# Kernel tuning notes

Hardware: AMD Instinct MI355X
Metric: run time of the kernel (lower is better)

Reference implementation:

```python
import jax, jax.numpy as jnp
import numpy as np

NUM_HEADS = 8
NUM_GROUPS = 32
EPS = 1e-5


def setup_inputs() -> dict:
    key = jax.random.key(0)
    ks = jax.random.split(key, 6)
    C = 512
    scale = 1.0 / np.sqrt(C)
    return {
        "q": jax.random.normal(ks[0], (2, C, 64, 64), dtype=jnp.float32),
        "gn_w": jnp.ones((C,), jnp.float32),
        "gn_b": jnp.zeros((C,), jnp.float32),
        "wq": jax.random.normal(ks[1], (C, C), jnp.float32) * scale,
        "bq": jnp.zeros((C,), jnp.float32),
        "wk": jax.random.normal(ks[2], (C, C), jnp.float32) * scale,
        "bk": jnp.zeros((C,), jnp.float32),
        "wv": jax.random.normal(ks[3], (C, C), jnp.float32) * scale,
        "bv": jnp.zeros((C,), jnp.float32),
        "wo": jax.random.normal(ks[4], (C, C), jnp.float32) * scale,
        "bo": jnp.zeros((C,), jnp.float32),
    }


def _group_norm(x, w, b):
    # x: [B, C, H, W]
    B, C, H, W = x.shape
    xg = x.reshape(B, NUM_GROUPS, C // NUM_GROUPS, H, W)
    mean = xg.mean(axis=(2, 3, 4), keepdims=True)
    var = xg.var(axis=(2, 3, 4), keepdims=True)
    xn = ((xg - mean) * jax.lax.rsqrt(var + EPS)).reshape(B, C, H, W)
    return xn * w[None, :, None, None] + b[None, :, None, None]


def reference(q, gn_w, gn_b, wq, bq, wk, bk, wv, bv, wo, bo):
    B, C, H, W = q.shape
    hd = C // NUM_HEADS
    resid = q
    x = _group_norm(q, gn_w, gn_b)
    x = x.reshape(B, C, H * W).transpose(0, 2, 1)  # [B, N, C]
    # torch Linear: y = x @ W.T + b  (self-attention: k = v = x)
    qp = x @ wq.T + bq
    kp = x @ wk.T + bk
    vp = x @ wv.T + bv
    N = H * W
    def split(t):  # [B, N, C] -> [B, h, N, hd]
        return t.reshape(B, N, NUM_HEADS, hd).transpose(0, 2, 1, 3)
    qh, kh, vh = split(qp), split(kp), split(vp)
    scores = jnp.einsum('bhnc,bhmc->bhnm', qh, kh) / jnp.sqrt(jnp.float32(hd))
    attn = jax.nn.softmax(scores, axis=-1)
    out = jnp.einsum('bhnm,bhmc->bhnc', attn, vh)
    out = out.transpose(0, 2, 1, 3).reshape(B, N, C)
    out = out @ wo.T + bo
    out2d = out.transpose(0, 2, 1).reshape(B, C, H, W)
    return out2d + resid
```

## Files before the change

kernel.cpp:

```cpp
#include <hip/hip_runtime.h>
#include <hip/hip_bf16.h>
#include <cstdint>
#include <cstddef>

using bf16x8   = __attribute__((ext_vector_type(8))) short;
using f32x4    = __attribute__((ext_vector_type(4))) float;
using f32x16   = __attribute__((ext_vector_type(16))) float;
using ushort8  = __attribute__((ext_vector_type(8))) unsigned short;
using ushort4v = __attribute__((ext_vector_type(4))) unsigned short;
using float4v  = __attribute__((ext_vector_type(4))) float;

#define MFMA16(a,b,c) __builtin_amdgcn_mfma_f32_16x16x32_bf16((a),(b),(c),0,0,0)
#define MFMA32(a,b,c) __builtin_amdgcn_mfma_f32_32x32x16_bf16((a),(b),(c),0,0,0)

#define QSCALE 0.18033688011112042f

__device__ __forceinline__ unsigned short f2bf(float f){
    union { float f; unsigned u; } v; v.f = f;
    unsigned r = v.u + 0x7FFFu + ((v.u >> 16) & 1u);
    return (unsigned short)(r >> 16);
}

__device__ __forceinline__ int cvtpk(float lo, float hi){
    int r;
    asm volatile("v_cvt_pk_bf16_f32 %0, %1, %2" : "=v"(r) : "v"(lo), "v"(hi));
    return r;
}

#if __has_builtin(__builtin_amdgcn_permlane32_swap)
__device__ __forceinline__ void plswap(int &a, int &b){
    auto r = __builtin_amdgcn_permlane32_swap(a, b, false, false);
    a = r[0]; b = r[1];
}
#else
__device__ __forceinline__ void plswap(int &a, int &b){
    int ta = __shfl_xor(a, 32), tb = __shfl_xor(b, 32);
    bool hi = ((threadIdx.x & 63) >= 32);
    int na = hi ? tb : a;
    int nb = hi ? b  : ta;
    a = na; b = nb;
}
#endif

__device__ __forceinline__ void gload16(const unsigned short* g, unsigned short* l){
    __builtin_amdgcn_global_load_lds(
        (const __attribute__((address_space(1))) void*)g,
        (__attribute__((address_space(3))) void*)l,
        16, 0, 0);
}

__global__ __launch_bounds__(256) void gn_stats_wconv(const float* __restrict__ x,
                                                      float* __restrict__ mean,
                                                      float* __restrict__ rstd,
                                                      const float* __restrict__ w0, const float* __restrict__ w1,
                                                      const float* __restrict__ w2, const float* __restrict__ w3,
                                                      unsigned short* wqk, unsigned short* wv, unsigned short* wo){
    int bid = blockIdx.x;
    if (bid < 64){
        int bg = bid;
        const float4v* p4 = (const float4v*)(x + (size_t)bg * 65536);
        float s = 0.f, ss = 0.f;
        for (int i = threadIdx.x; i < 16384; i += 256){
            float4v v = p4[i];
            s  += v[0]+v[1]+v[2]+v[3];
            ss += v[0]*v[0]+v[1]*v[1]+v[2]*v[2]+v[3]*v[3];
        }
        __shared__ float ls[4], lss[4];
        int lane = threadIdx.x & 63, w = threadIdx.x >> 6;
        #pragma unroll
        for (int o = 32; o > 0; o >>= 1){ s += __shfl_down(s, o); ss += __shfl_down(ss, o); }
        if (lane == 0){ ls[w] = s; lss[w] = ss; }
        __syncthreads();
        if (threadIdx.x == 0){
            float S = ls[0]+ls[1]+ls[2]+ls[3];
            float SS = lss[0]+lss[1]+lss[2]+lss[3];
            float m = S * (1.f/65536.f);
            float var = SS * (1.f/65536.f) - m*m;
            mean[bg] = m;
            rstd[bg] = rsqrtf(var + 1e-5f);
        }
    } else {
        int i2 = bid - 64;
        int y = i2 >> 8, bx = i2 & 255;
        const float* src; unsigned short* dst; float sc = 1.0f;
        switch (y){
            case 0: src = w0; dst = wqk;          sc = QSCALE; break;
            case 1: src = w1; dst = wqk + 512*512; break;
            case 2: src = w2; dst = wv; break;
            default: src = w3; dst = wo; break;
        }
        int i = (bx*256 + threadIdx.x) * 4;
        float4v v = *(const float4v*)(src + i);
        ushort4v o;
        #pragma unroll
        for (int j = 0; j < 4; j++) o[j] = f2bf(v[j]*sc);
        *(ushort4v*)(dst + i) = o;
    }
}

__global__ __launch_bounds__(256) void gn_apply(const float* __restrict__ x,
                                                const float* __restrict__ mean,
                                                const float* __restrict__ rstd,
                                                const float* __restrict__ gw,
                                                const float* __restrict__ gb,
                                                unsigned short* __restrict__ xn){
    int b = blockIdx.z, c0 = blockIdx.y * 64, n0 = blockIdx.x * 64;
    __shared__ unsigned short tile[64][68];
    for (int i = threadIdx.x; i < 64*16; i += 256){
        int row = i >> 4, f4 = i & 15;
        int c = c0 + row;
        int g = b*32 + (c >> 4);
        float rs = rstd[g];
        float wgt = gw[c] * rs;
        float bia = gb[c] - mean[g] * wgt;
        float4v v = *(const float4v*)(x + ((size_t)(b*512 + c))*4096 + n0 + f4*4);
        ushort4v o;
        #pragma unroll
        for (int j = 0; j < 4; j++) o[j] = f2bf(v[j]*wgt + bia);
        *(ushort4v*)&tile[row][f4*4] = o;
    }
    __syncthreads();
    for (int i = threadIdx.x; i < 64*8; i += 256){
        int nr = i >> 3, c8 = i & 7;
        ushort8 o;
        #pragma unroll
        for (int j = 0; j < 8; j++) o[j] = tile[c8*8 + j][nr];
        *(ushort8*)(xn + ((size_t)(b*4096 + n0 + nr))*512 + c0 + c8*8) = o;
    }
}

__global__ __launch_bounds__(256) void gemm_qkv(const unsigned short* __restrict__ xn,
                                                const unsigned short* __restrict__ wqk,
                                                const unsigned short* __restrict__ Wv,
                                                const float* __restrict__ bq,
                                                const float* __restrict__ bk,
                                                const float* __restrict__ bv,
                                                unsigned short* __restrict__ Q,
                                                unsigned short* __restrict__ K,
                                                unsigned short* __restrict__ Vt){
    __shared__ unsigned short Al[128*32];
    __shared__ unsigned short Bl[128*32];
    int bid = blockIdx.x;
    int t = threadIdx.x, lane = t & 63, w = t >> 6;
    int wr = w >> 1, wc = w & 1;
    int lr = lane >> 2, lc = lane & 3;

    if (bid < 512){
        int m0 = (bid & 63) * 128, n0 = (bid >> 6) * 128;
        f32x4 acc[4][4] = {};
        const unsigned short* Asrc = xn  + (size_t)(m0 + w*32 + lr)*512 + lc*8;
        const unsigned short* Bsrc = wqk + (size_t)(n0 + w*32 + lr)*512 + lc*8;
        unsigned short* Adst = &Al[(w*32)*32];
        unsigned short* Bdst = &Bl[(w*32)*32];

        for (int ks = 0; ks < 16; ks++){
            gload16(Asrc + ks*32,          Adst);
            gload16(Asrc + ks*32 + 16*512, Adst + 16*32);
            gload16(Bsrc + ks*32,          Bdst);
            gload16(Bsrc + ks*32 + 16*512, Bdst + 16*32);
            asm volatile("s_waitcnt vmcnt(0)" ::: "memory");
            __syncthreads();
            bf16x8 a[4], b[4];
            #pragma unroll
            for (int mi = 0; mi < 4; mi++) a[mi] = *(bf16x8*)&Al[(wr*64 + mi*16 + (lane&15))*32 + (lane>>4)*8];
            #pragma unroll
            for (int ni = 0; ni < 4; ni++) b[ni] = *(bf16x8*)&Bl[(wc*64 + ni*16 + (lane&15))*32 + (lane>>4)*8];
            #pragma unroll
            for (int mi = 0; mi < 4; mi++)
                #pragma unroll
                for (int ni = 0; ni < 4; ni++)
                    acc[mi][ni] = MFMA16(a[mi], b[ni], acc[mi][ni]);
            __syncthreads();
        }

        int cK = n0 >> 9;
        const float* bias = cK ? bk : bq;
        unsigned short* dst0 = cK ? K : Q;
        float bsc = cK ? 1.0f : QSCALE;
        #pragma unroll
        for (int mi = 0; mi < 4; mi++)
            #pragma unroll
            for (int ni = 0; ni < 4; ni++)
                #pragma unroll
                for (int r = 0; r < 4; r++){
                    int mrow = m0 + wr*64 + mi*16 + (lane>>4)*4 + r;
                    int col  = (n0 & 511) + wc*64 + ni*16 + (lane&15);
                    int b_ = mrow >> 12, n = mrow & 4095;
                    int h = col >> 6, d = col & 63;
                    float v = acc[mi][ni][r] + bias[col]*bsc;
                    dst0[(size_t)((b_*8+h)*4096 + n)*64 + d] = f2bf(v);
                }
    } else {
        int i2 = bid - 512;
        int m0 = (i2 & 7) * 64, n0 = (i2 >> 3) * 128;
        f32x4 acc[2][4] = {};
        const unsigned short* Asrc = Wv + (size_t)(m0 + w*16 + lr)*512 + lc*8;
        const unsigned short* Bsrc = xn + (size_t)(n0 + w*32 + lr)*512 + lc*8;
        unsigned short* Adst = &Al[(w*16)*32];
        unsigned short* Bdst = &Bl[(w*32)*32];

        for (int ks = 0; ks < 16; ks++){
            gload16(Asrc + ks*32,          Adst);
            gload16(Bsrc + ks*32,          Bdst);
            gload16(Bsrc + ks*32 + 16*512, Bdst + 16*32);
            asm volatile("s_waitcnt vmcnt(0)" ::: "memory");
            __syncthreads();
            bf16x8 a[2], b[4];
            #pragma unroll
            for (int mi = 0; mi < 2; mi++) a[mi] = *(bf16x8*)&Al[(wr*32 + mi*16 + (lane&15))*32 + (lane>>4)*8];
            #pragma unroll
            for (int ni = 0; ni < 4; ni++) b[ni] = *(bf16x8*)&Bl[(wc*64 + ni*16 + (lane&15))*32 + (lane>>4)*8];
            #pragma unroll
            for (int mi = 0; mi < 2; mi++)
                #pragma unroll
                for (int ni = 0; ni < 4; ni++)
                    acc[mi][ni] = MFMA16(a[mi], b[ni], acc[mi][ni]);
            __syncthreads();
        }
        #pragma unroll
        for (int mi = 0; mi < 2; mi++)
            #pragma unroll
            for (int ni = 0; ni < 4; ni++)
                #pragma unroll
                for (int r = 0; r < 4; r++){
                    int row  = m0 + wr*32 + mi*16 + (lane>>4)*4 + r;
                    int colm = n0 + wc*64 + ni*16 + (lane&15);
                    int b_ = colm >> 12, n = colm & 4095;
                    int h = row >> 6, d = row & 63;
                    float v = acc[mi][ni][r] + bv[row];
                    Vt[(size_t)((b_*8+h)*64 + d)*4096 + n] = f2bf(v);
                }
    }
}

__global__ __launch_bounds__(256) void gemm_o2(const unsigned short* __restrict__ Wo,
                                               const unsigned short* __restrict__ Om,
                                               const float* __restrict__ bo,
                                               const float* __restrict__ resid,
                                               float* __restrict__ outp){
    __shared__ unsigned short Al[64*32];
    __shared__ unsigned short Bl[128*32];
    int t = threadIdx.x, lane = t & 63, w = t >> 6;
    int wr = w >> 1, wc = w & 1;
    int m0 = blockIdx.x * 64, n0 = blockIdx.y * 128;
    int lr = lane >> 2, lc = lane & 3;
    f32x4 acc[2][4] = {};

    const unsigned short* Asrc = Wo + (size_t)(m0 + w*16 + lr)*512 + lc*8;
    const unsigned short* Bsrc = Om + (size_t)(n0 + w*32 + lr)*512 + lc*8;
    unsigned short* Adst = &Al[(w*16)*32];
    unsigned short* Bdst = &Bl[(w*32)*32];

    for (int ks = 0; ks < 16; ks++){
        gload16(Asrc + ks*32,          Adst);
        gload16(Bsrc + ks*32,          Bdst);
        gload16(Bsrc + ks*32 + 16*512, Bdst + 16*32);
        asm volatile("s_waitcnt vmcnt(0)" ::: "memory");
        __syncthreads();
        bf16x8 a[2], b[4];
        #pragma unroll
        for (int mi = 0; mi < 2; mi++) a[mi] = *(bf16x8*)&Al[(wr*32 + mi*16 + (lane&15))*32 + (lane>>4)*8];
        #pragma unroll
        for (int ni = 0; ni < 4; ni++) b[ni] = *(bf16x8*)&Bl[(wc*64 + ni*16 + (lane&15))*32 + (lane>>4)*8];
        #pragma unroll
        for (int mi = 0; mi < 2; mi++)
            #pragma unroll
            for (int ni = 0; ni < 4; ni++)
                acc[mi][ni] = MFMA16(a[mi], b[ni], acc[mi][ni]);
        __syncthreads();
    }
    #pragma unroll
    for (int mi = 0; mi < 2; mi++)
        #pragma unroll
        for (int ni = 0; ni < 4; ni++)
            #pragma unroll
            for (int r = 0; r < 4; r++){
                int row  = m0 + wr*32 + mi*16 + (lane>>4)*4 + r;
                int colm = n0 + wc*64 + ni*16 + (lane&15);
                int b_ = colm >> 12, n = colm & 4095;
                size_t oi = ((size_t)(b_*512 + row))*4096 + n;
                outp[oi] = acc[mi][ni][r] + bo[row] + resid[oi];
            }
}

__global__ __launch_bounds__(128, 2) void attn5(const unsigned short* __restrict__ Q,
                                                const unsigned short* __restrict__ K,
                                                const unsigned short* __restrict__ Vt,
                                                unsigned short* __restrict__ O){
    int bid = blockIdx.x;
    int idx = bid >> 3;
    int bh = ((bid & 7) << 1) | (idx >> 6);
    int qt = idx & 63;
    int t = threadIdx.x, lane = t & 63, w = t >> 6;
    int ln = lane & 31, hi = lane >> 5;
    int q0 = qt * 64;

    __shared__ unsigned short Kl[2][64*64];
    __shared__ unsigned short Vl[2][64*64];

    const unsigned short* Qb = Q  + (size_t)bh * 4096 * 64;
    const unsigned short* Kb = K  + (size_t)bh * 4096 * 64;
    const unsigned short* Vb = Vt + (size_t)bh * 64 * 4096;

    bf16x8 bqa[4], bqb[4];
    #pragma unroll
    for (int dsub = 0; dsub < 4; dsub++){
        bqa[dsub] = *(const bf16x8*)(Qb + (size_t)(q0 + ln)*64      + dsub*16 + hi*8);
        bqb[dsub] = *(const bf16x8*)(Qb + (size_t)(q0 + 32 + ln)*64 + dsub*16 + hi*8);
    }

    int srow = lane >> 3;
    int sswz = (lane & 7) ^ srow;

    auto stage = [&](int buf, int kt){
        int kv0 = kt * 64;
        #pragma unroll
        for (int i = 0; i < 4; i++){
            int r0 = w*32 + i*8;
            gload16(Kb + (size_t)(kv0 + r0 + srow)*64 + sswz*8, &Kl[buf][r0*64]);
        }
        #pragma unroll
        for (int i = 0; i < 4; i++){
            int r0 = w*32 + i*8;
            gload16(Vb + (size_t)(r0 + srow)*4096 + kv0 + sswz*8, &Vl[buf][r0*64]);
        }
    };

    stage(0, 0);

    f32x16 o0a, o1a, o0b, o1b, z;
    #pragma unroll
    for (int r = 0; r < 16; r++){ o0a[r]=0.f; o1a[r]=0.f; o0b[r]=0.f; o1b[r]=0.f; z[r]=0.f; }
    float lsA = 0.f, lsB = 0.f;

    const char* KbA = (const char*)&Kl[0][0] + (w*32 + ln)*128;
    const char* VbA = (const char*)&Vl[0][0] + ln*128;
    int swzr = (ln & 7) << 4;

    for (int kt = 0; kt < 64; kt++){
        asm volatile("s_waitcnt vmcnt(0)" ::: "memory");
        __builtin_amdgcn_s_barrier();
        __builtin_amdgcn_sched_barrier(0);
        if (kt < 63) stage((kt + 1) & 1, kt + 1);
        __builtin_amdgcn_sched_barrier(0);

        int boff = (kt & 1) * (64*64*2);

        f32x16 sA, sB;
        {
            int cb = (hi*16) ^ swzr;
            bf16x8 ak = *(const bf16x8*)(KbA + boff + cb);
            sA = MFMA32(ak, bqa[0], z);
            sB = MFMA32(ak, bqb[0], z);
        }
        __builtin_amdgcn_s_setprio(1);
        #pragma unroll
        for (int dsub = 1; dsub < 4; dsub++){
            int cb = (dsub*32 + hi*16) ^ swzr;
            bf16x8 ak = *(const bf16x8*)(KbA + boff + cb);
            sA = MFMA32(ak, bqa[dsub], sA);
            sB = MFMA32(ak, bqb[dsub], sB);
        }
        __builtin_amdgcn_s_setprio(0);

        #pragma unroll
        for (int r = 0; r < 16; r++){ sA[r] = __builtin_amdgcn_exp2f(sA[r]); lsA += sA[r]; }
        #pragma unroll
        for (int r = 0; r < 16; r++){ sB[r] = __builtin_amdgcn_exp2f(sB[r]); lsB += sB[r]; }

        __builtin_amdgcn_s_setprio(1);
        #pragma unroll
        for (int hsel = 0; hsel < 2; hsel++){
            int obp = hsel * 8;
            int a0 = cvtpk(sA[obp+0], sA[obp+1]);
            int a1 = cvtpk(sA[obp+2], sA[obp+3]);
            int c0 = cvtpk(sA[obp+4], sA[obp+5]);
            int c1 = cvtpk(sA[obp+6], sA[obp+7]);
            plswap(a0, c0);
            plswap(a1, c1);
            union { int i[4]; bf16x8 v; } fuA;
            fuA.i[0] = a0; fuA.i[1] = a1; fuA.i[2] = c0; fuA.i[3] = c1;

            int d0 = cvtpk(sB[obp+0], sB[obp+1]);
            int d1 = cvtpk(sB[obp+2], sB[obp+3]);
            int e0 = cvtpk(sB[obp+4], sB[obp+5]);
            int e1 = cvtpk(sB[obp+6], sB[obp+7]);
            plswap(d0, e0);
            plswap(d1, e1);
            union { int i[4]; bf16x8 v; } fuB;
            fuB.i[0] = d0; fuB.i[1] = d1; fuB.i[2] = e0; fuB.i[3] = e1;

            int cb = ((w*4 + hsel*2 + hi) << 4) ^ swzr;
            bf16x8 av0 = *(const bf16x8*)(VbA + boff + cb);
            bf16x8 av1 = *(const bf16x8*)(VbA + boff + 32*128 + cb);
            o0a = MFMA32(av0, fuA.v, o0a);
            o1a = MFMA32(av1, fuA.v, o1a);
            o0b = MFMA32(av0, fuB.v, o0b);
            o1b = MFMA32(av1, fuB.v, o1b);
        }
        __builtin_amdgcn_s_setprio(0);
    }

    lsA += __shfl_xor(lsA, 32);
    lsB += __shfl_xor(lsB, 32);
    __syncthreads();
    float* m1 = (float*)&Kl[0][0];
    float* m2 = (float*)&Vl[0][0];
    if (w == 1){
        #pragma unroll
        for (int r = 0; r < 16; r++){
            m1[r*64 + lane]        = o0a[r];
            m1[1024 + r*64 + lane] = o1a[r];
            m2[r*64 + lane]        = o0b[r];
            m2[1024 + r*64 + lane] = o1b[r];
        }
        if (hi == 0){ m2[2048 + ln] = lsA; m2[2048 + 32 + ln] = lsB; }
    }
    __syncthreads();
    if (w == 0){
        #pragma unroll
        for (int r = 0; r < 16; r++){
            o0a[r] += m1[r*64 + lane];
            o1a[r] += m1[1024 + r*64 + lane];
            o0b[r] += m2[r*64 + lane];
            o1b[r] += m2[1024 + r*64 + lane];
        }
        float rA = 1.0f / (lsA + m2[2048 + ln]);
        float rB = 1.0f / (lsB + m2[2048 + 32 + ln]);
        int b = bh >> 3, h = bh & 7;
        unsigned short* dstA = O + (size_t)(b*4096 + q0 + ln)*512      + h*64;
        unsigned short* dstB = O + (size_t)(b*4096 + q0 + 32 + ln)*512 + h*64;
        #pragma unroll
        for (int m = 0; m < 2; m++){
            const f32x16& ovA = m ? o1a : o0a;
            const f32x16& ovB = m ? o1b : o0b;
            #pragma unroll
            for (int g = 0; g < 4; g++){
                int d = m*32 + g*8 + hi*4;
                ushort4v pkA, pkB;
                #pragma unroll
                for (int j = 0; j < 4; j++){
                    pkA[j] = f2bf(ovA[g*4 + j] * rA);
                    pkB[j] = f2bf(ovB[g*4 + j] * rB);
                }
                *(ushort4v*)(dstA + d) = pkA;
                *(ushort4v*)(dstB + d) = pkB;
            }
        }
    }
}

extern "C" void kernel_launch(void* const* d_in, const int* in_sizes, int n_in,
                              void* d_out, int out_size, void* d_ws, size_t ws_size,
                              hipStream_t stream) {
    const float* q    = (const float*)d_in[0];
    const float* gn_w = (const float*)d_in[1];
    const float* gn_b = (const float*)d_in[2];
    const float* wq   = (const float*)d_in[3];
    const float* bq   = (const float*)d_in[4];
    const float* wk   = (const float*)d_in[5];
    const float* bk   = (const float*)d_in[6];
    const float* wv   = (const float*)d_in[7];
    const float* bv   = (const float*)d_in[8];
    const float* wo   = (const float*)d_in[9];
    const float* bo   = (const float*)d_in[10];
    float* outp = (float*)d_out;

    char* ws = (char*)d_ws;
    float* mean = (float*)ws;
    float* rstd = (float*)(ws + 256);
    unsigned short* xn  = (unsigned short*)(ws + 1024);
    const size_t TOK = (size_t)8192 * 512;
    unsigned short* wqkb = xn + TOK;
    unsigned short* wvb  = wqkb + 1024*512;
    unsigned short* wob  = wvb + 512*512;
    unsigned short* Qb   = wob + 512*512;
    unsigned short* Kb   = Qb + TOK;
    unsigned short* Vt   = Kb + TOK;
    unsigned short* Ob   = Vt + TOK;

    gn_stats_wconv<<<1088, 256, 0, stream>>>(q, mean, rstd, wq, wk, wv, wo, wqkb, wvb, wob);
    gn_apply<<<dim3(64, 8, 2), 256, 0, stream>>>(q, mean, rstd, gn_w, gn_b, xn);
    gemm_qkv<<<1024, 256, 0, stream>>>(xn, wqkb, wvb, bq, bk, bv, Qb, Kb, Vt);
    attn5<<<1024, 128, 0, stream>>>(Qb, Kb, Vt, Ob);
    gemm_o2<<<dim3(8, 64), 256, 0, stream>>>(wob, Ob, bo, q, outp);
}
```

Baseline: 156.2 us.

## Split attention KV range four ways with separate merge kernel

Adds a split-KV attention kernel in which each single-wave block handles 64 queries over a quarter of the keys. It writes unnormalized bf16 partial outputs and row sums, and a merge kernel then adds the partials and normalizes. This raises the block count from 1024 to 4096 to improve occupancy and latency hiding, at the cost of extra workspace traffic and a fourth launch. The path runs only when the workspace is large enough, otherwise it falls back to attn5. The V-projection and output-projection GEMM block index orders are also swapped, which changes which blocks run together and so cache reuse.

Result: slower. 170.6 us (+9.2%).

```diff
diff --git a/kernel.cpp b/kernel.cpp
--- a/kernel.cpp
+++ b/kernel.cpp
@@ -192,7 +192,7 @@
                 }
     } else {
         int i2 = bid - 512;
-        int m0 = (i2 & 7) * 64, n0 = (i2 >> 3) * 128;
+        int m0 = (i2 >> 6) * 64, n0 = (i2 & 63) * 128;
         f32x4 acc[2][4] = {};
         const unsigned short* Asrc = Wv + (size_t)(m0 + w*16 + lr)*512 + lc*8;
         const unsigned short* Bsrc = xn + (size_t)(n0 + w*32 + lr)*512 + lc*8;
@@ -242,7 +242,7 @@
     __shared__ unsigned short Bl[128*32];
     int t = threadIdx.x, lane = t & 63, w = t >> 6;
     int wr = w >> 1, wc = w & 1;
-    int m0 = blockIdx.x * 64, n0 = blockIdx.y * 128;
+    int m0 = blockIdx.y * 64, n0 = blockIdx.x * 128;
     int lr = lane >> 2, lc = lane & 3;
     f32x4 acc[2][4] = {};
 
@@ -281,6 +281,192 @@
                 size_t oi = ((size_t)(b_*512 + row))*4096 + n;
                 outp[oi] = acc[mi][ni][r] + bo[row] + resid[oi];
             }
+}
+
+__global__ __launch_bounds__(64, 3) void attn8(const unsigned short* __restrict__ Q,
+                                               const unsigned short* __restrict__ K,
+                                               const unsigned short* __restrict__ Vt,
+                                               unsigned short* __restrict__ Opart,
+                                               float* __restrict__ Lpart){
+    int bid = blockIdx.x;
+    int xcd = bid & 7;
+    int idx = bid >> 3;
+    int bh  = (xcd << 1) | (idx >> 8);
+    int rest = idx & 255;
+    int qt = rest >> 2;
+    int kq = rest & 3;
+    int lane = threadIdx.x & 63;
+    int ln = lane & 31, hi = lane >> 5;
+    int q0 = qt * 64;
+    int kvbase = kq * 1024;
+
+    __shared__ unsigned short Kl[2][32*64];
+    __shared__ unsigned short Vl[32*64];
+
+    const unsigned short* Qb = Q  + (size_t)bh * 4096 * 64;
+    const unsigned short* Kb = K  + (size_t)bh * 4096 * 64;
+    const unsigned short* Vb = Vt + (size_t)bh * 64 * 4096;
+
+    bf16x8 bqa[4], bqb[4];
+    #pragma unroll
+    for (int dsub = 0; dsub < 4; dsub++){
+        bqa[dsub] = *(const bf16x8*)(Qb + (size_t)(q0 + ln)*64      + dsub*16 + hi*8);
+        bqb[dsub] = *(const bf16x8*)(Qb + (size_t)(q0 + 32 + ln)*64 + dsub*16 + hi*8);
+    }
+
+    int srow = lane >> 3;
+    int sswz = (lane & 7) ^ srow;
+    int vd   = (srow << 1) + (sswz >> 2);
+    int vkvo = (sswz & 3) * 8;
+
+    auto stageK = [&](int kt){
+        int kv0 = kvbase + kt*32;
+        unsigned short* dst = &Kl[kt & 1][0];
+        #pragma unroll
+        for (int i = 0; i < 4; i++)
+            gload16(Kb + (size_t)(kv0 + i*8 + srow)*64 + sswz*8, dst + i*512);
+    };
+    auto stageV = [&](int kt){
+        int kv0 = kvbase + kt*32;
+        #pragma unroll
+        for (int i = 0; i < 4; i++)
+            gload16(Vb + (size_t)(vd + i*16)*4096 + kv0 + vkvo, &Vl[i*512]);
+    };
+
+    f32x16 o0a, o1a, o0b, o1b, z;
+    #pragma unroll
+    for (int r = 0; r < 16; r++){ o0a[r]=0.f; o1a[r]=0.f; o0b[r]=0.f; o1b[r]=0.f; z[r]=0.f; }
+    float lsA = 0.f, lsB = 0.f;
+
+    const char* Kbase0 = (const char*)&Kl[0][0] + ln*128;
+    const char* Vbase0 = (const char*)&Vl[0];
+    int kswz  = ln & 7;
+    int vrow  = (ln >> 1) * 128;
+    int vswzr = (ln >> 1) & 7;
+    int vlnb  = (ln & 1) << 2;
+
+    stageK(0);
+    stageV(0);
+    stageK(1);
+
+    for (int kt = 0; kt < 32; kt++){
+        if (kt < 31) asm volatile("s_waitcnt vmcnt(4)" ::: "memory");
+        else         asm volatile("s_waitcnt vmcnt(0)" ::: "memory");
+        __builtin_amdgcn_sched_barrier(0);
+        int boff = (kt & 1) * (32*64*2);
+
+        f32x16 sA, sB;
+        {
+            bf16x8 ak = *(const bf16x8*)(Kbase0 + boff + ((hi ^ kswz) << 4));
+            sA = MFMA32(ak, bqa[0], z);
+            sB = MFMA32(ak, bqb[0], z);
+        }
+        __builtin_amdgcn_s_setprio(1);
+        #pragma unroll
+        for (int dsub = 1; dsub < 4; dsub++){
+            bf16x8 ak = *(const bf16x8*)(Kbase0 + boff + ((((dsub<<1)|hi) ^ kswz) << 4));
+            sA = MFMA32(ak, bqa[dsub], sA);
+            sB = MFMA32(ak, bqb[dsub], sB);
+        }
+        __builtin_amdgcn_s_setprio(0);
+
+        #pragma unroll
+        for (int r = 0; r < 16; r++){ sA[r] = __builtin_amdgcn_exp2f(sA[r]); lsA += sA[r]; }
+        #pragma unroll
+        for (int r = 0; r < 16; r++){ sB[r] = __builtin_amdgcn_exp2f(sB[r]); lsB += sB[r]; }
+
+        __builtin_amdgcn_s_setprio(1);
+        #pragma unroll
+        for (int ksub = 0; ksub < 2; ksub++){
+            int obp = ksub * 8;
+            int a0 = cvtpk(sA[obp+0], sA[obp+1]);
+            int a1 = cvtpk(sA[obp+2], sA[obp+3]);
+            int c0 = cvtpk(sA[obp+4], sA[obp+5]);
+            int c1 = cvtpk(sA[obp+6], sA[obp+7]);
+            plswap(a0, c0); plswap(a1, c1);
+            union { int i[4]; bf16x8 v; } fuA;
+            fuA.i[0] = a0; fuA.i[1] = a1; fuA.i[2] = c0; fuA.i[3] = c1;
+
+            int d0 = cvtpk(sB[obp+0], sB[obp+1]);
+            int d1 = cvtpk(sB[obp+2], sB[obp+3]);
+            int e0 = cvtpk(sB[obp+4], sB[obp+5]);
+            int e1 = cvtpk(sB[obp+6], sB[obp+7]);
+            plswap(d0, e0); plswap(d1, e1);
+            union { int i[4]; bf16x8 v; } fuB;
+            fuB.i[0] = d0; fuB.i[1] = d1; fuB.i[2] = e0; fuB.i[3] = e1;
+
+            int vs = (((vlnb | (ksub<<1) | hi) ^ vswzr) << 4);
+            bf16x8 av0 = *(const bf16x8*)(Vbase0 + vrow + vs);
+            bf16x8 av1 = *(const bf16x8*)(Vbase0 + 16*128 + vrow + vs);
+            o0a = MFMA32(av0, fuA.v, o0a);
+            o1a = MFMA32(av1, fuA.v, o1a);
+            o0b = MFMA32(av0, fuB.v, o0b);
+            o1b = MFMA32(av1, fuB.v, o1b);
+        }
+        __builtin_amdgcn_s_setprio(0);
+
+        __builtin_amdgcn_sched_barrier(0);
+        if (kt < 31) stageV(kt + 1);
+        if (kt < 30) stageK(kt + 2);
+        __builtin_amdgcn_sched_barrier(0);
+    }
+
+    lsA += __shfl_xor(lsA, 32);
+    lsB += __shfl_xor(lsB, 32);
+    size_t obase = ((size_t)(kq*16 + bh))*4096 + q0;
+    if (hi == 0){
+        Lpart[obase + ln]      = lsA;
+        Lpart[obase + 32 + ln] = lsB;
+    }
+    unsigned short* dA = Opart + (obase + ln)*64;
+    unsigned short* dB = Opart + (obase + 32 + ln)*64;
+    #pragma unroll
+    for (int m = 0; m < 2; m++){
+        const f32x16& ovA = m ? o1a : o0a;
+        const f32x16& ovB = m ? o1b : o0b;
+        #pragma unroll
+        for (int g = 0; g < 4; g++){
+            int d = m*32 + g*8 + hi*4;
+            ushort4v pkA, pkB;
+            #pragma unroll
+            for (int j = 0; j < 4; j++){
+                pkA[j] = f2bf(ovA[g*4 + j]);
+                pkB[j] = f2bf(ovB[g*4 + j]);
+            }
+            *(ushort4v*)(dA + d) = pkA;
+            *(ushort4v*)(dB + d) = pkB;
+        }
+    }
+}
+
+__global__ __launch_bounds__(256) void attn_merge(const unsigned short* __restrict__ Op,
+                                                  const float* __restrict__ Lp,
+                                                  unsigned short* __restrict__ Om){
+    int g = blockIdx.x*256 + threadIdx.x;
+    int token = g >> 6;
+    int cc = g & 63;
+    int h = cc >> 3, dd = (cc & 7)*8;
+    int b = token >> 12, n = token & 4095;
+    int bh = b*8 + h;
+    float acc[8] = {};
+    float l = 0.f;
+    #pragma unroll
+    for (int kq = 0; kq < 4; kq++){
+        size_t row = ((size_t)(kq*16 + bh))*4096 + n;
+        ushort8 ov = *(const ushort8*)(Op + row*64 + dd);
+        #pragma unroll
+        for (int j = 0; j < 8; j++){
+            union { unsigned u; float f; } cv;
+            cv.u = ((unsigned)(unsigned short)ov[j]) << 16;
+            acc[j] += cv.f;
+        }
+        l += Lp[row];
+    }
+    float r = 1.0f / l;
+    ushort8 o;
+    #pragma unroll
+    for (int j = 0; j < 8; j++) o[j] = f2bf(acc[j]*r);
+    *(ushort8*)(Om + (size_t)token*512 + h*64 + dd) = o;
 }
 
 __global__ __launch_bounds__(128, 2) void attn5(const unsigned short* __restrict__ Q,
@@ -478,10 +664,20 @@
     unsigned short* Kb   = Qb + TOK;
     unsigned short* Vt   = Kb + TOK;
     unsigned short* Ob   = Vt + TOK;
+    unsigned short* Opart = Ob + TOK;
+    float* Lpart = (float*)(Opart + 4*TOK);
+
+    size_t need = (size_t)(Opart - xn + 4*TOK)*2 + 1024 + 262144*4;
+    bool big = ws_size >= need;
 
     gn_stats_wconv<<<1088, 256, 0, stream>>>(q, mean, rstd, wq, wk, wv, wo, wqkb, wvb, wob);
     gn_apply<<<dim3(64, 8, 2), 256, 0, stream>>>(q, mean, rstd, gn_w, gn_b, xn);
     gemm_qkv<<<1024, 256, 0, stream>>>(xn, wqkb, wvb, bq, bk, bv, Qb, Kb, Vt);
-    attn5<<<1024, 128, 0, stream>>>(Qb, Kb, Vt, Ob);
-    gemm_o2<<<dim3(8, 64), 256, 0, stream>>>(wob, Ob, bo, q, outp);
-}
+    if (big){
+        attn8<<<4096, 64, 0, stream>>>(Qb, Kb, Vt, Opart, Lpart);
+        attn_merge<<<2048, 256, 0, stream>>>(Opart, Lpart, Ob);
+    } else {
+        attn5<<<1024, 128, 0, stream>>>(Qb, Kb, Vt, Ob);
+    }
+    gemm_o2<<<dim3(64, 8), 256, 0, stream>>>(wob, Ob, bo, q, outp);
+}
```

## Split group-norm stats into partial sums and reorder GEMM block rasterization

Applied to the files above, without the earlier changes.

The group-norm statistics pass now uses 512 blocks, each summing 8192 elements into partial sum and sum-of-squares pairs, instead of 64 blocks each scanning a full group. gn_apply finishes the per-group reduction itself from 8 partials before normalizing. This is meant to fill the GPU during the bandwidth-bound stats pass. The V-projection and output-projection GEMMs also swap their block-index mapping so consecutive blocks share the same weight tile, which changes cache reuse patterns.

Result: faster. 135.1 us (-13.5%).

```diff
diff --git a/kernel.cpp b/kernel.cpp
--- a/kernel.cpp
+++ b/kernel.cpp
@@ -9,6 +9,7 @@
 using ushort8  = __attribute__((ext_vector_type(8))) unsigned short;
 using ushort4v = __attribute__((ext_vector_type(4))) unsigned short;
 using float4v  = __attribute__((ext_vector_type(4))) float;
+using float2v  = __attribute__((ext_vector_type(2))) float;
 
 #define MFMA16(a,b,c) __builtin_amdgcn_mfma_f32_16x16x32_bf16((a),(b),(c),0,0,0)
 #define MFMA32(a,b,c) __builtin_amdgcn_mfma_f32_32x32x16_bf16((a),(b),(c),0,0,0)
@@ -50,18 +51,17 @@
 }
 
 __global__ __launch_bounds__(256) void gn_stats_wconv(const float* __restrict__ x,
-                                                      float* __restrict__ mean,
-                                                      float* __restrict__ rstd,
+                                                      float2v* __restrict__ parts,
                                                       const float* __restrict__ w0, const float* __restrict__ w1,
                                                       const float* __restrict__ w2, const float* __restrict__ w3,
                                                       unsigned short* wqk, unsigned short* wv, unsigned short* wo){
     int bid = blockIdx.x;
-    if (bid < 64){
-        int bg = bid;
-        const float4v* p4 = (const float4v*)(x + (size_t)bg * 65536);
+    if (bid < 512){
+        const float4v* p4 = (const float4v*)(x + (size_t)bid * 8192);
         float s = 0.f, ss = 0.f;
-        for (int i = threadIdx.x; i < 16384; i += 256){
-            float4v v = p4[i];
+        #pragma unroll
+        for (int i = 0; i < 8; i++){
+            float4v v = p4[i*256 + threadIdx.x];
             s  += v[0]+v[1]+v[2]+v[3];
             ss += v[0]*v[0]+v[1]*v[1]+v[2]*v[2]+v[3]*v[3];
         }
@@ -72,15 +72,13 @@
         if (lane == 0){ ls[w] = s; lss[w] = ss; }
         __syncthreads();
         if (threadIdx.x == 0){
-            float S = ls[0]+ls[1]+ls[2]+ls[3];
-            float SS = lss[0]+lss[1]+lss[2]+lss[3];
-            float m = S * (1.f/65536.f);
-            float var = SS * (1.f/65536.f) - m*m;
-            mean[bg] = m;
-            rstd[bg] = rsqrtf(var + 1e-5f);
+            float2v p;
+            p[0] = ls[0]+ls[1]+ls[2]+ls[3];
+            p[1] = lss[0]+lss[1]+lss[2]+lss[3];
+            parts[bid] = p;
         }
     } else {
-        int i2 = bid - 64;
+        int i2 = bid - 512;
         int y = i2 >> 8, bx = i2 & 255;
         const float* src; unsigned short* dst; float sc = 1.0f;
         switch (y){
@@ -99,20 +97,34 @@
 }
 
 __global__ __launch_bounds__(256) void gn_apply(const float* __restrict__ x,
-                                                const float* __restrict__ mean,
-                                                const float* __restrict__ rstd,
+                                                const float2v* __restrict__ parts,
                                                 const float* __restrict__ gw,
                                                 const float* __restrict__ gb,
                                                 unsigned short* __restrict__ xn){
     int b = blockIdx.z, c0 = blockIdx.y * 64, n0 = blockIdx.x * 64;
     __shared__ unsigned short tile[64][68];
+    __shared__ float gmean[4], grstd[4];
+    if (threadIdx.x < 4){
+        int g = b*32 + (c0 >> 4) + threadIdx.x;
+        float s = 0.f, ss = 0.f;
+        #pragma unroll
+        for (int e = 0; e < 8; e++){
+            float2v p = parts[g*8 + e];
+            s += p[0]; ss += p[1];
+        }
+        float m = s * (1.f/65536.f);
+        float var = ss * (1.f/65536.f) - m*m;
+        gmean[threadIdx.x] = m;
+        grstd[threadIdx.x] = rsqrtf(var + 1e-5f);
+    }
+    __syncthreads();
     for (int i = threadIdx.x; i < 64*16; i += 256){
         int row = i >> 4, f4 = i & 15;
         int c = c0 + row;
-        int g = b*32 + (c >> 4);
-        float rs = rstd[g];
+        int gl = row >> 4;
+        float rs = grstd[gl];
         float wgt = gw[c] * rs;
-        float bia = gb[c] - mean[g] * wgt;
+        float bia = gb[c] - gmean[gl] * wgt;
         float4v v = *(const float4v*)(x + ((size_t)(b*512 + c))*4096 + n0 + f4*4);
         ushort4v o;
         #pragma unroll
@@ -192,7 +204,7 @@
                 }
     } else {
         int i2 = bid - 512;
-        int m0 = (i2 & 7) * 64, n0 = (i2 >> 3) * 128;
+        int m0 = (i2 >> 6) * 64, n0 = (i2 & 63) * 128;
         f32x4 acc[2][4] = {};
         const unsigned short* Asrc = Wv + (size_t)(m0 + w*16 + lr)*512 + lc*8;
         const unsigned short* Bsrc = xn + (size_t)(n0 + w*32 + lr)*512 + lc*8;
@@ -242,7 +254,7 @@
     __shared__ unsigned short Bl[128*32];
     int t = threadIdx.x, lane = t & 63, w = t >> 6;
     int wr = w >> 1, wc = w & 1;
-    int m0 = blockIdx.x * 64, n0 = blockIdx.y * 128;
+    int m0 = blockIdx.y * 64, n0 = blockIdx.x * 128;
     int lr = lane >> 2, lc = lane & 3;
     f32x4 acc[2][4] = {};
 
@@ -467,9 +479,8 @@
     float* outp = (float*)d_out;
 
     char* ws = (char*)d_ws;
-    float* mean = (float*)ws;
-    float* rstd = (float*)(ws + 256);
-    unsigned short* xn  = (unsigned short*)(ws + 1024);
+    float2v* parts = (float2v*)ws;
+    unsigned short* xn  = (unsigned short*)(ws + 8192);
     const size_t TOK = (size_t)8192 * 512;
     unsigned short* wqkb = xn + TOK;
     unsigned short* wvb  = wqkb + 1024*512;
@@ -479,9 +490,9 @@
     unsigned short* Vt   = Kb + TOK;
     unsigned short* Ob   = Vt + TOK;
 
-    gn_stats_wconv<<<1088, 256, 0, stream>>>(q, mean, rstd, wq, wk, wv, wo, wqkb, wvb, wob);
-    gn_apply<<<dim3(64, 8, 2), 256, 0, stream>>>(q, mean, rstd, gn_w, gn_b, xn);
+    gn_stats_wconv<<<1536, 256, 0, stream>>>(q, parts, wq, wk, wv, wo, wqkb, wvb, wob);
+    gn_apply<<<dim3(64, 8, 2), 256, 0, stream>>>(q, parts, gn_w, gn_b, xn);
     gemm_qkv<<<1024, 256, 0, stream>>>(xn, wqkb, wvb, bq, bk, bv, Qb, Kb, Vt);
     attn5<<<1024, 128, 0, stream>>>(Qb, Kb, Vt, Ob);
-    gemm_o2<<<dim3(8, 64), 256, 0, stream>>>(wob, Ob, bo, q, outp);
-}
+    gemm_o2<<<dim3(64, 8), 256, 0, stream>>>(wob, Ob, bo, q, outp);
+}
```
